# Performance work log

Hardware: AMD Instinct MI355X
Metric: run time of the kernel (lower is better)

Reference implementation:

```python
import jax, jax.numpy as jnp
import numpy as np

N, L, T, D = 64, 196, 32, 512


def setup_inputs() -> dict:
    key = jax.random.key(0)
    ks = jax.random.split(key, 12)
    s = 1.0 / np.sqrt(D)
    return {
        "feature_1": jax.random.normal(ks[0], (N, L, D), jnp.float32),
        "feature_2": jax.random.normal(ks[1], (N, T, D), jnp.float32),
        "w_att": jax.random.normal(ks[2], (D,), jnp.float32) * s,
        "b_att": jnp.zeros((), jnp.float32),
        "n1_w1": jax.random.normal(ks[3], (D, D), jnp.float32) * s,
        "n1_b1": jnp.zeros((D,), jnp.float32),
        "n1_w2": jax.random.normal(ks[4], (D, D), jnp.float32) * s,
        "n1_b2": jnp.zeros((D,), jnp.float32),
        "n2_w1": jax.random.normal(ks[5], (D, D), jnp.float32) * s,
        "n2_b1": jnp.zeros((D,), jnp.float32),
        "n2_w2": jax.random.normal(ks[6], (D, D), jnp.float32) * s,
        "n2_b2": jnp.zeros((D,), jnp.float32),
    }


def _glu(x, w1, b1, w2, b2):
    # tanh(Linear1(x)) * sigmoid(Linear2(x))
    return jnp.tanh(x @ w1 + b1) * jax.nn.sigmoid(x @ w2 + b2)


def reference(feature_1, feature_2, w_att, b_att,
              n1_w1, n1_b1, n1_w2, n1_b2,
              n2_w1, n2_b1, n2_w2, n2_b2):
    f1_emb = _glu(feature_1, n1_w1, n1_b1, n1_w2, n1_b2)  # [N,L,D]
    f2_emb = _glu(feature_2, n2_w1, n2_b1, n2_w2, n2_b2)  # [N,T,D]
    # Attention_1: fc((f1 + f2 broadcast)) == fc(f1) + fc(f2) + bias since fc is linear.
    # Avoids materializing the [N,T,L,D] intermediate while computing identical math.
    s1 = feature_1 @ w_att  # [N,L]
    s2 = feature_2 @ w_att  # [N,T]
    att_logits = s2[:, :, None] + s1[:, None, :] + b_att  # [N,T,L]
    att = jax.nn.softmax(att_logits, axis=2)
    f_hat = jnp.einsum('ntl,nld->ntd', att, feature_1)  # [N,T,D]
    return (f2_emb + f_hat, f1_emb, att)
```

## Files before the change

kernel.cpp:

```cpp
#include <hip/hip_runtime.h>
#include <hip/hip_bf16.h>
#include <cstdint>
#include <cstddef>

#define N_  64
#define L_  196
#define T_  32
#define D_  512
#define LP_ 256
#define ROWS1_ (N_ * L_)
#define ROWS2_ (N_ * T_)
#define MT1_   (ROWS1_ / 128)
#define NWG1_  (MT1_ * 4)
#define NWG2_  ((ROWS2_ / 128) * 4)

typedef __attribute__((ext_vector_type(8))) short short8;
typedef __attribute__((ext_vector_type(4))) float f32x4;

__device__ inline unsigned short f2bf(float f) {
  unsigned u = __builtin_bit_cast(unsigned, f);
  u = u + 0x7FFFu + ((u >> 16) & 1u);
  return (unsigned short)(u >> 16);
}

__global__ __launch_bounds__(256)
void cvt_dots(const float* __restrict__ f1, const float* __restrict__ f2,
              const float* __restrict__ w,
              unsigned short* __restrict__ f1b, unsigned short* __restrict__ f2b,
              float* __restrict__ s1, float* __restrict__ s2) {
  int row = blockIdx.x * 4 + (threadIdx.x >> 6);
  int lane = threadIdx.x & 63;
  bool isf1 = row < ROWS1_;
  const float* src = isf1 ? (f1 + (size_t)row * D_) : (f2 + (size_t)(row - ROWS1_) * D_);
  unsigned short* dst = isf1 ? (f1b + (size_t)row * D_) : (f2b + (size_t)(row - ROWS1_) * D_);
  float4 x0 = ((const float4*)src)[lane];
  float4 x1 = ((const float4*)src)[lane + 64];
  float4 w0 = ((const float4*)w)[lane];
  float4 w1 = ((const float4*)w)[lane + 64];
  float d = x0.x * w0.x + x0.y * w0.y + x0.z * w0.z + x0.w * w0.w
          + x1.x * w1.x + x1.y * w1.y + x1.z * w1.z + x1.w * w1.w;
  ushort4 o0, o1;
  o0.x = f2bf(x0.x); o0.y = f2bf(x0.y); o0.z = f2bf(x0.z); o0.w = f2bf(x0.w);
  o1.x = f2bf(x1.x); o1.y = f2bf(x1.y); o1.z = f2bf(x1.z); o1.w = f2bf(x1.w);
  ((ushort4*)dst)[lane] = o0;
  ((ushort4*)dst)[lane + 64] = o1;
  #pragma unroll
  for (int s = 32; s; s >>= 1) d += __shfl_xor(d, s);
  if (lane == 0) {
    if (isf1) s1[row] = d; else s2[row - ROWS1_] = d;
  }
}

__global__ __launch_bounds__(256)
void wt_cvt(const float* __restrict__ w0, const float* __restrict__ w1,
            const float* __restrict__ w2, const float* __restrict__ w3,
            unsigned short* __restrict__ o0, unsigned short* __restrict__ o1,
            unsigned short* __restrict__ o2, unsigned short* __restrict__ o3) {
  const float* W = (blockIdx.y == 0) ? w0 : (blockIdx.y == 1) ? w1 : (blockIdx.y == 2) ? w2 : w3;
  unsigned short* O = (blockIdx.y == 0) ? o0 : (blockIdx.y == 1) ? o1 : (blockIdx.y == 2) ? o2 : o3;
  int k0 = (blockIdx.x >> 3) * 64, n0 = (blockIdx.x & 7) * 64;
  __shared__ float tl[64][65];
  int t = threadIdx.x;
  #pragma unroll
  for (int i = 0; i < 16; i++) {
    int e = t + i * 256;
    int r = e >> 6, c = e & 63;
    tl[r][c] = W[(size_t)(k0 + r) * D_ + n0 + c];
  }
  __syncthreads();
  #pragma unroll
  for (int i = 0; i < 16; i++) {
    int e = t + i * 256;
    int r = e >> 6, c = e & 63;
    O[(size_t)(n0 + r) * D_ + k0 + c] = f2bf(tl[c][r]);
  }
}

__global__ __launch_bounds__(256)
void f1t_cvt(const float* __restrict__ f1, unsigned short* __restrict__ f1t) {
  int bi = blockIdx.x;
  int n = bi >> 5, rem = bi & 31;
  int l0 = (rem >> 3) * 64, d0 = (rem & 7) * 64;
  __shared__ float tl[64][65];
  int t = threadIdx.x;
  #pragma unroll
  for (int i = 0; i < 16; i++) {
    int e = t + i * 256;
    int r = e >> 6, c = e & 63;
    int l = l0 + r;
    tl[r][c] = (l < L_) ? f1[((size_t)n * L_ + l) * D_ + d0 + c] : 0.f;
  }
  __syncthreads();
  #pragma unroll
  for (int i = 0; i < 16; i++) {
    int e = t + i * 256;
    int r = e >> 6, c = e & 63;
    f1t[((size_t)n * D_ + d0 + r) * LP_ + l0 + c] = f2bf(tl[c][r]);
  }
}

__global__ __launch_bounds__(64)
void softmax_att(const float* __restrict__ s1, const float* __restrict__ s2,
                 const float* __restrict__ b_att, float* __restrict__ att,
                 unsigned short* __restrict__ attb) {
  int b = blockIdx.x;
  int n = b >> 5;
  int lane = threadIdx.x;
  float s2v = s2[b] + b_att[0];
  const float* s1n = s1 + (size_t)n * L_;
  float v[4];
  float mx = -1e30f;
  #pragma unroll
  for (int j = 0; j < 4; j++) {
    int l = lane + j * 64;
    v[j] = (l < L_) ? (s1n[l] + s2v) : -1e30f;
    mx = fmaxf(mx, v[j]);
  }
  #pragma unroll
  for (int s = 32; s; s >>= 1) mx = fmaxf(mx, __shfl_xor(mx, s));
  float sum = 0.f;
  #pragma unroll
  for (int j = 0; j < 4; j++) { v[j] = __expf(v[j] - mx); sum += v[j]; }
  #pragma unroll
  for (int s = 32; s; s >>= 1) sum += __shfl_xor(sum, s);
  float inv = 1.f / sum;
  float* an = att + (size_t)b * L_;
  unsigned short* ab = attb + (size_t)b * LP_;
  #pragma unroll
  for (int j = 0; j < 4; j++) {
    int l = lane + j * 64;
    float p = v[j] * inv;
    if (l < L_) an[l] = p;
    ab[l] = (l < L_) ? f2bf(p) : (unsigned short)0;
  }
}

__global__ __launch_bounds__(256, 2)
void glu_gemm(const unsigned short* __restrict__ Xb1, const unsigned short* __restrict__ Xb2,
              const unsigned short* __restrict__ W1t_1, const unsigned short* __restrict__ W2t_1,
              const unsigned short* __restrict__ W1t_2, const unsigned short* __restrict__ W2t_2,
              const float* __restrict__ b1_1, const float* __restrict__ b2_1,
              const float* __restrict__ b1_2, const float* __restrict__ b2_2,
              float* __restrict__ o1, float* __restrict__ o0) {
  int nwg = gridDim.x;
  int q = nwg >> 3;
  int orig = blockIdx.x;
  int bid = (orig & 7) * q + (orig >> 3);
  const unsigned short *Xb, *W1t, *W2t;
  const float *b1, *b2;
  float* out;
  if (bid < NWG1_) { Xb = Xb1; W1t = W1t_1; W2t = W2t_1; b1 = b1_1; b2 = b2_1; out = o1; }
  else { bid -= NWG1_; Xb = Xb2; W1t = W1t_2; W2t = W2t_2; b1 = b1_2; b2 = b2_2; out = o0; }
  int nt = bid & 3, mt = bid >> 2;
  int m0 = mt * 128, n0 = nt * 128;
  int t = threadIdx.x, lane = t & 63, wave = t >> 6;
  int wr = (wave >> 1) * 64, wc = (wave & 1) * 64;

  __shared__ alignas(16) unsigned short Xs[2][4096];
  __shared__ alignas(16) unsigned short Ws[2][2][4096];

  auto stage = [&](int buf, int k0) {
    #pragma unroll
    for (int i = 0; i < 2; i++) {
      int c = t + i * 256;
      const unsigned short* g = Xb + (size_t)(m0 + (c >> 2)) * D_ + k0 + (c & 3) * 8;
      unsigned short* l = &Xs[buf][(size_t)(wave * 64 + i * 256) * 8];
      __builtin_amdgcn_global_load_lds((const __attribute__((address_space(1))) unsigned int*)g,
                                       (__attribute__((address_space(3))) unsigned int*)l,
                                       16, 0, 0);
    }
    #pragma unroll
    for (int w = 0; w < 2; w++) {
      const unsigned short* Wt = w ? W2t : W1t;
      #pragma unroll
      for (int i = 0; i < 2; i++) {
        int c = t + i * 256;
        const unsigned short* g = Wt + (size_t)(n0 + (c >> 2)) * D_ + k0 + (c & 3) * 8;
        unsigned short* l = &Ws[buf][w][(size_t)(wave * 64 + i * 256) * 8];
        __builtin_amdgcn_global_load_lds((const __attribute__((address_space(1))) unsigned int*)g,
                                         (__attribute__((address_space(3))) unsigned int*)l,
                                         16, 0, 0);
      }
    }
  };

  f32x4 acc1[4][4], acc2[4][4];
  #pragma unroll
  for (int i = 0; i < 4; i++)
    #pragma unroll
    for (int j = 0; j < 4; j++) { acc1[i][j] = (f32x4)(0.f); acc2[i][j] = (f32x4)(0.f); }

  stage(0, 0);
  int cur = 0;
  int arow = lane & 15, ak = (lane >> 4) * 8;
  for (int ks = 0; ks < 16; ++ks) {
    __syncthreads();
    if (ks < 15) stage(cur ^ 1, (ks + 1) * 32);
    short8 a[4], bf1[4], bf2[4];
    #pragma unroll
    for (int mf = 0; mf < 4; mf++)
      a[mf] = *(const short8*)&Xs[cur][(wr + mf * 16 + arow) * 32 + ak];
    #pragma unroll
    for (int nf = 0; nf < 4; nf++) {
      bf1[nf] = *(const short8*)&Ws[cur][0][(wc + nf * 16 + arow) * 32 + ak];
      bf2[nf] = *(const short8*)&Ws[cur][1][(wc + nf * 16 + arow) * 32 + ak];
    }
    #pragma unroll
    for (int mf = 0; mf < 4; mf++)
      #pragma unroll
      for (int nf = 0; nf < 4; nf++) {
        acc1[mf][nf] = __builtin_amdgcn_mfma_f32_16x16x32_bf16(a[mf], bf1[nf], acc1[mf][nf], 0, 0, 0);
        acc2[mf][nf] = __builtin_amdgcn_mfma_f32_16x16x32_bf16(a[mf], bf2[nf], acc2[mf][nf], 0, 0, 0);
      }
    cur ^= 1;
  }

  int crow = (lane >> 4) * 4, ccol = lane & 15;
  #pragma unroll
  for (int mf = 0; mf < 4; mf++) {
    #pragma unroll
    for (int nf = 0; nf < 4; nf++) {
      int col = n0 + wc + nf * 16 + ccol;
      float bb1 = b1[col], bb2 = b2[col];
      #pragma unroll
      for (int r = 0; r < 4; r++) {
        int row = m0 + wr + mf * 16 + crow + r;
        float z1 = acc1[mf][nf][r] + bb1;
        float z2 = acc2[mf][nf][r] + bb2;
        float th = 1.f - 2.f / (__expf(2.f * z1) + 1.f);
        float sg = 1.f / (1.f + __expf(-z2));
        out[(size_t)row * D_ + col] = th * sg;
      }
    }
  }
}

__global__ __launch_bounds__(256)
void fhat_mfma(const unsigned short* __restrict__ attb,
               const unsigned short* __restrict__ f1t,
               float* __restrict__ out0) {
  int n = blockIdx.x >> 2, dq = blockIdx.x & 3;
  int lane = threadIdx.x & 63, wave = threadIdx.x >> 6;
  int d0 = dq * 128 + wave * 32;
  int arow = lane & 15, ak = (lane >> 4) * 8;
  const unsigned short* A = attb + (size_t)n * T_ * LP_;
  const unsigned short* B = f1t + ((size_t)n * D_ + d0) * LP_;
  f32x4 acc[2][2];
  #pragma unroll
  for (int i = 0; i < 2; i++)
    #pragma unroll
    for (int j = 0; j < 2; j++) acc[i][j] = (f32x4)(0.f);
  #pragma unroll 2
  for (int kk = 0; kk < 8; kk++) {
    int k0 = kk * 32;
    short8 a[2], b[2];
    #pragma unroll
    for (int mt = 0; mt < 2; mt++)
      a[mt] = *(const short8*)&A[(size_t)(mt * 16 + arow) * LP_ + k0 + ak];
    #pragma unroll
    for (int nt2 = 0; nt2 < 2; nt2++)
      b[nt2] = *(const short8*)&B[(size_t)(nt2 * 16 + arow) * LP_ + k0 + ak];
    #pragma unroll
    for (int mt = 0; mt < 2; mt++)
      #pragma unroll
      for (int nt2 = 0; nt2 < 2; nt2++)
        acc[mt][nt2] = __builtin_amdgcn_mfma_f32_16x16x32_bf16(a[mt], b[nt2], acc[mt][nt2], 0, 0, 0);
  }
  int crow = (lane >> 4) * 4, ccol = lane & 15;
  #pragma unroll
  for (int mt = 0; mt < 2; mt++) {
    #pragma unroll
    for (int nt2 = 0; nt2 < 2; nt2++) {
      int d = d0 + nt2 * 16 + ccol;
      #pragma unroll
      for (int r = 0; r < 4; r++) {
        int tt = mt * 16 + crow + r;
        size_t idx = ((size_t)n * T_ + tt) * D_ + d;
        out0[idx] += acc[mt][nt2][r];
      }
    }
  }
}

extern "C" void kernel_launch(void* const* d_in, const int* in_sizes, int n_in,
                              void* d_out, int out_size, void* d_ws, size_t ws_size,
                              hipStream_t stream) {
  const float* f1    = (const float*)d_in[0];
  const float* f2    = (const float*)d_in[1];
  const float* w_att = (const float*)d_in[2];
  const float* b_att = (const float*)d_in[3];
  const float* n1w1  = (const float*)d_in[4];
  const float* n1b1  = (const float*)d_in[5];
  const float* n1w2  = (const float*)d_in[6];
  const float* n1b2  = (const float*)d_in[7];
  const float* n2w1  = (const float*)d_in[8];
  const float* n2b1  = (const float*)d_in[9];
  const float* n2w2  = (const float*)d_in[10];
  const float* n2b2  = (const float*)d_in[11];

  float* out0 = (float*)d_out;
  float* out1 = out0 + (size_t)N_ * T_ * D_;
  float* att  = out1 + (size_t)N_ * L_ * D_;

  char* ws = (char*)d_ws;
  auto alloc = [&](size_t bytes) { char* p = ws; ws += (bytes + 255) & ~(size_t)255; return p; };
  unsigned short* f1b   = (unsigned short*)alloc((size_t)ROWS1_ * D_ * 2);
  unsigned short* f2b   = (unsigned short*)alloc((size_t)ROWS2_ * D_ * 2);
  unsigned short* w1t_1 = (unsigned short*)alloc((size_t)D_ * D_ * 2);
  unsigned short* w2t_1 = (unsigned short*)alloc((size_t)D_ * D_ * 2);
  unsigned short* w1t_2 = (unsigned short*)alloc((size_t)D_ * D_ * 2);
  unsigned short* w2t_2 = (unsigned short*)alloc((size_t)D_ * D_ * 2);
  unsigned short* f1t   = (unsigned short*)alloc((size_t)N_ * D_ * LP_ * 2);
  unsigned short* attb  = (unsigned short*)alloc((size_t)N_ * T_ * LP_ * 2);
  float* s1 = (float*)alloc((size_t)ROWS1_ * 4);
  float* s2 = (float*)alloc((size_t)ROWS2_ * 4);

  cvt_dots<<<(ROWS1_ + ROWS2_) / 4, 256, 0, stream>>>(f1, f2, w_att, f1b, f2b, s1, s2);
  wt_cvt<<<dim3(64, 4), 256, 0, stream>>>(n1w1, n1w2, n2w1, n2w2, w1t_1, w2t_1, w1t_2, w2t_2);
  glu_gemm<<<NWG1_ + NWG2_, 256, 0, stream>>>(f1b, f2b, w1t_1, w2t_1, w1t_2, w2t_2,
                                              n1b1, n1b2, n2b1, n2b2, out1, out0);
  f1t_cvt<<<N_ * 32, 256, 0, stream>>>(f1, f1t);
  softmax_att<<<N_ * T_, 64, 0, stream>>>(s1, s2, b_att, att, attb);
  fhat_mfma<<<N_ * 4, 256, 0, stream>>>(attb, f1t, out0);
}
```

Before: 152.5 us.

## Halve GLU GEMM M-tile to 64 and transpose f1 from bf16 copy

The GLU GEMM now uses 64-row M tiles instead of 128. That doubles the workgroup count and halves the accumulator registers, with occupancy raised to 3 blocks per CU, to improve load balance and latency hiding. The cost is more redundant reads of the weight tiles. Separately, the f1 transpose kernel now reads the bf16 copy already produced by cvt_dots and moves data in 4-element vectors, cutting its global read traffic in half.

```diff
diff --git a/kernel.cpp b/kernel.cpp
--- a/kernel.cpp
+++ b/kernel.cpp
@@ -10,9 +10,8 @@
 #define LP_ 256
 #define ROWS1_ (N_ * L_)
 #define ROWS2_ (N_ * T_)
-#define MT1_   (ROWS1_ / 128)
-#define NWG1_  (MT1_ * 4)
-#define NWG2_  ((ROWS2_ / 128) * 4)
+#define NWG1_  ((ROWS1_ / 64) * 4)
+#define NWG2_  ((ROWS2_ / 64) * 4)
 
 typedef __attribute__((ext_vector_type(8))) short short8;
 typedef __attribute__((ext_vector_type(4))) float f32x4;
@@ -77,25 +76,33 @@
 }
 
 __global__ __launch_bounds__(256)
-void f1t_cvt(const float* __restrict__ f1, unsigned short* __restrict__ f1t) {
+void f1t_cvt(const unsigned short* __restrict__ f1b, unsigned short* __restrict__ f1t) {
   int bi = blockIdx.x;
   int n = bi >> 5, rem = bi & 31;
   int l0 = (rem >> 3) * 64, d0 = (rem & 7) * 64;
-  __shared__ float tl[64][65];
+  __shared__ unsigned short tl[64][72];
   int t = threadIdx.x;
   #pragma unroll
-  for (int i = 0; i < 16; i++) {
+  for (int i = 0; i < 4; i++) {
     int e = t + i * 256;
-    int r = e >> 6, c = e & 63;
+    int r = e >> 4, c4 = e & 15;
     int l = l0 + r;
-    tl[r][c] = (l < L_) ? f1[((size_t)n * L_ + l) * D_ + d0 + c] : 0.f;
+    ushort4 v;
+    if (l < L_) v = *(const ushort4*)&f1b[((size_t)n * L_ + l) * D_ + d0 + c4 * 4];
+    else { v.x = 0; v.y = 0; v.z = 0; v.w = 0; }
+    *(ushort4*)&tl[r][c4 * 4] = v;
   }
   __syncthreads();
   #pragma unroll
-  for (int i = 0; i < 16; i++) {
+  for (int i = 0; i < 4; i++) {
     int e = t + i * 256;
-    int r = e >> 6, c = e & 63;
-    f1t[((size_t)n * D_ + d0 + r) * LP_ + l0 + c] = f2bf(tl[c][r]);
+    int r = e >> 4, c4 = e & 15;
+    ushort4 o;
+    o.x = tl[c4 * 4 + 0][r];
+    o.y = tl[c4 * 4 + 1][r];
+    o.z = tl[c4 * 4 + 2][r];
+    o.w = tl[c4 * 4 + 3][r];
+    *(ushort4*)&f1t[((size_t)n * D_ + d0 + r) * LP_ + l0 + c4 * 4] = o;
   }
 }
 
@@ -135,7 +142,7 @@
   }
 }
 
-__global__ __launch_bounds__(256, 2)
+__global__ __launch_bounds__(256, 3)
 void glu_gemm(const unsigned short* __restrict__ Xb1, const unsigned short* __restrict__ Xb2,
               const unsigned short* __restrict__ W1t_1, const unsigned short* __restrict__ W2t_1,
               const unsigned short* __restrict__ W1t_2, const unsigned short* __restrict__ W2t_2,
@@ -152,19 +159,18 @@
   if (bid < NWG1_) { Xb = Xb1; W1t = W1t_1; W2t = W2t_1; b1 = b1_1; b2 = b2_1; out = o1; }
   else { bid -= NWG1_; Xb = Xb2; W1t = W1t_2; W2t = W2t_2; b1 = b1_2; b2 = b2_2; out = o0; }
   int nt = bid & 3, mt = bid >> 2;
-  int m0 = mt * 128, n0 = nt * 128;
+  int m0 = mt * 64, n0 = nt * 128;
   int t = threadIdx.x, lane = t & 63, wave = t >> 6;
-  int wr = (wave >> 1) * 64, wc = (wave & 1) * 64;
-
-  __shared__ alignas(16) unsigned short Xs[2][4096];
+  int wr = (wave >> 1) * 32, wc = (wave & 1) * 64;
+
+  __shared__ alignas(16) unsigned short Xs[2][2048];
   __shared__ alignas(16) unsigned short Ws[2][2][4096];
 
   auto stage = [&](int buf, int k0) {
-    #pragma unroll
-    for (int i = 0; i < 2; i++) {
-      int c = t + i * 256;
+    {
+      int c = t;
       const unsigned short* g = Xb + (size_t)(m0 + (c >> 2)) * D_ + k0 + (c & 3) * 8;
-      unsigned short* l = &Xs[buf][(size_t)(wave * 64 + i * 256) * 8];
+      unsigned short* l = &Xs[buf][(size_t)wave * 512];
       __builtin_amdgcn_global_load_lds((const __attribute__((address_space(1))) unsigned int*)g,
                                        (__attribute__((address_space(3))) unsigned int*)l,
                                        16, 0, 0);
@@ -184,9 +190,9 @@
     }
   };
 
-  f32x4 acc1[4][4], acc2[4][4];
-  #pragma unroll
-  for (int i = 0; i < 4; i++)
+  f32x4 acc1[2][4], acc2[2][4];
+  #pragma unroll
+  for (int i = 0; i < 2; i++)
     #pragma unroll
     for (int j = 0; j < 4; j++) { acc1[i][j] = (f32x4)(0.f); acc2[i][j] = (f32x4)(0.f); }
 
@@ -196,9 +202,9 @@
   for (int ks = 0; ks < 16; ++ks) {
     __syncthreads();
     if (ks < 15) stage(cur ^ 1, (ks + 1) * 32);
-    short8 a[4], bf1[4], bf2[4];
-    #pragma unroll
-    for (int mf = 0; mf < 4; mf++)
+    short8 a[2], bf1[4], bf2[4];
+    #pragma unroll
+    for (int mf = 0; mf < 2; mf++)
       a[mf] = *(const short8*)&Xs[cur][(wr + mf * 16 + arow) * 32 + ak];
     #pragma unroll
     for (int nf = 0; nf < 4; nf++) {
@@ -206,7 +212,7 @@
       bf2[nf] = *(const short8*)&Ws[cur][1][(wc + nf * 16 + arow) * 32 + ak];
     }
     #pragma unroll
-    for (int mf = 0; mf < 4; mf++)
+    for (int mf = 0; mf < 2; mf++)
       #pragma unroll
       for (int nf = 0; nf < 4; nf++) {
         acc1[mf][nf] = __builtin_amdgcn_mfma_f32_16x16x32_bf16(a[mf], bf1[nf], acc1[mf][nf], 0, 0, 0);
@@ -217,7 +223,7 @@
 
   int crow = (lane >> 4) * 4, ccol = lane & 15;
   #pragma unroll
-  for (int mf = 0; mf < 4; mf++) {
+  for (int mf = 0; mf < 2; mf++) {
     #pragma unroll
     for (int nf = 0; nf < 4; nf++) {
       int col = n0 + wc + nf * 16 + ccol;
@@ -319,7 +325,7 @@
   wt_cvt<<<dim3(64, 4), 256, 0, stream>>>(n1w1, n1w2, n2w1, n2w2, w1t_1, w2t_1, w1t_2, w2t_2);
   glu_gemm<<<NWG1_ + NWG2_, 256, 0, stream>>>(f1b, f2b, w1t_1, w2t_1, w1t_2, w2t_2,
                                               n1b1, n1b2, n2b1, n2b2, out1, out0);
-  f1t_cvt<<<N_ * 32, 256, 0, stream>>>(f1, f1t);
+  f1t_cvt<<<N_ * 32, 256, 0, stream>>>(f1b, f1t);
   softmax_att<<<N_ * T_, 64, 0, stream>>>(s1, s2, b_att, att, attb);
   fhat_mfma<<<N_ * 4, 256, 0, stream>>>(attb, f1t, out0);
 }
```

Result: slower. 157.9 us (+3.6%).
